# Performance work log

Measured on AMD Instinct MI355X. Metric: run time of the kernel, lower is better.

## Reference

```python
import jax, jax.numpy as jnp
import numpy as np

NUM_FEAT = 10
GAMMA = 1.0
HIDDEN = 30


def setup_inputs() -> dict:
    key = jax.random.key(0)
    ks = jax.random.split(key, 10)
    B, T = 2048, 512
    atom_i = jax.random.randint(ks[0], (B, T), 0, 118, dtype=jnp.int32)
    atom_j = jax.random.randint(ks[1], (B, T), 0, 118, dtype=jnp.int32)
    dist = jax.random.uniform(ks[2], (B, T), minval=0.5, maxval=7.0, dtype=jnp.float32)
    emb = jax.random.normal(ks[3], (118, NUM_FEAT), dtype=jnp.float32)
    s = 1.0 / np.sqrt(HIDDEN)
    W_ih = jax.random.uniform(ks[4], (3 * HIDDEN, NUM_FEAT), minval=-s, maxval=s, dtype=jnp.float32)
    W_hh = jax.random.uniform(ks[5], (3 * HIDDEN, HIDDEN), minval=-s, maxval=s, dtype=jnp.float32)
    b_ih = jax.random.uniform(ks[6], (3 * HIDDEN,), minval=-s, maxval=s, dtype=jnp.float32)
    b_hh = jax.random.uniform(ks[7], (3 * HIDDEN,), minval=-s, maxval=s, dtype=jnp.float32)
    W_out = jax.random.uniform(ks[8], (1, HIDDEN), minval=-s, maxval=s, dtype=jnp.float32)
    b_out = jax.random.uniform(ks[9], (1,), minval=-s, maxval=s, dtype=jnp.float32)
    return dict(atom_i=atom_i, atom_j=atom_j, dist=dist, emb=emb,
                W_ih=W_ih, W_hh=W_hh, b_ih=b_ih, b_hh=b_hh,
                W_out=W_out, b_out=b_out)


def _forward(atom_i, atom_j, dist, emb, W_ih, W_hh, b_ih, b_hh, W_out, b_out):
    B = atom_i.shape[0]
    mask_i = (atom_i != 0)[..., None]  # [B,T,1]
    mask_j = (atom_j != 0)[..., None]
    # conditional embedding gather: index 0 means 'no atom' -> zero vector
    e_i = jnp.where(mask_i, emb[atom_i], 0.0)  # [B,T,10]
    e_j = jnp.where(mask_j, emb[atom_j], 0.0)
    # RBF distance expansion, zeroed where atom_i is absent
    centers = jnp.arange(1, NUM_FEAT + 1, dtype=dist.dtype) * 0.7  # [10]
    rbf = jnp.exp(-GAMMA * (centers - dist[..., None]) ** 2)  # [B,T,10]
    rbf = jnp.where(mask_i, rbf, 0.0)
    feat = jnp.concatenate([e_i, e_j, rbf], axis=-1)  # [B,T,30]
    # view(B,10,-1).permute(0,2,1): row-major reshape then transpose -> [B, 3T, 10]
    x = feat.reshape(B, NUM_FEAT, -1).transpose(0, 2, 1)
    # GRU (batch_first, 1 layer); precompute input projections for all steps
    gi = jnp.einsum('bsd,hd->bsh', x, W_ih) + b_ih  # [B, 3T, 90]

    def step(h, g):
        gh = h @ W_hh.T + b_hh  # [B,90]
        i_r, i_z, i_n = jnp.split(g, 3, axis=-1)
        h_r, h_z, h_n = jnp.split(gh, 3, axis=-1)
        r = jax.nn.sigmoid(i_r + h_r)
        z = jax.nn.sigmoid(i_z + h_z)
        n = jnp.tanh(i_n + r * h_n)
        h = (1.0 - z) * n + z * h
        return h, None

    h0 = jnp.zeros((B, HIDDEN), dtype=x.dtype)
    h_last, _ = jax.lax.scan(step, h0, gi.transpose(1, 0, 2))  # only last step is used
    # dropout is identity in eval mode
    out = jax.nn.relu(h_last @ W_out.T + b_out)  # [B,1]
    return out.squeeze(-1)  # [B]


def reference(atom_i, atom_j, dist, emb, W_ih, W_hh, b_ih, b_hh, W_out, b_out):
    return _forward(atom_i, atom_j, dist, emb, W_ih, W_hh, b_ih, b_hh, W_out, b_out)
```

## Files before the change

kernel.cpp:

```cpp
#include <hip/hip_runtime.h>

#define BATCH 2048
#define T 512
#define NF 10
#define HID 30
#define S3T 1536
#define FEAT_PER_B 15360

typedef float v2f __attribute__((ext_vector_type(2)));

#define LOG2E 1.44269504088896f

__device__ __forceinline__ float fexp(float x) {
    return __builtin_amdgcn_exp2f(x * LOG2E);
}
__device__ __forceinline__ float frcp(float x) {
    return __builtin_amdgcn_rcpf(x);
}

__device__ __forceinline__ v2f pk_fma(v2f a, v2f b, v2f c) {
    v2f d;
    asm("v_pk_fma_f32 %0, %1, %2, %3" : "=v"(d) : "v"(a), "v"(b), "v"(c));
    return d;
}

__global__ void __launch_bounds__(512)
feat_kernel(const int* __restrict__ atom_i,
            const int* __restrict__ atom_j,
            const float* __restrict__ dist,
            const float* __restrict__ emb,
            float4* __restrict__ xpair4) {
    __shared__ float lf[512 * 31 + 30];
    const int b = blockIdx.x;
    const int t = threadIdx.x;

    {
        const int bt = b * T + t;
        const int ai = atom_i[bt];
        const int aj = atom_j[bt];
        const float dd = dist[bt];
        const float mi = (ai != 0) ? 1.0f : 0.0f;
        const float mj = (aj != 0) ? 1.0f : 0.0f;
        const float* ei = &emb[ai * NF];
        const float* ej = &emb[aj * NF];
        float* row = &lf[t * 31];
#pragma unroll
        for (int c = 0; c < NF; ++c) row[c] = mi * ei[c];
#pragma unroll
        for (int c = 0; c < NF; ++c) row[10 + c] = mj * ej[c];
#pragma unroll
        for (int c = 0; c < NF; ++c) {
            float ctr = (float)(c + 1) * 0.7f;
            float df = ctr - dd;
            row[20 + c] = mi * fexp(-df * df);
        }
    }
    __syncthreads();

    float4* ob = xpair4 + (long)b * (FEAT_PER_B / 4);
    for (int o = t; o < FEAT_PER_B / 4; o += 512) {
        unsigned p  = (unsigned)o / 768u;
        unsigned c4 = (unsigned)o - p * 768u;
        float vv[4];
#pragma unroll
        for (int kx = 0; kx < 4; ++kx) {
            unsigned s = 2u * c4 + (unsigned)(kx >> 1);
            unsigned e = (unsigned)(kx & 1);
            unsigned f = (2u * p + e) * 1536u + s;
            unsigned tt = f / 30u;
            unsigned cc = f - tt * 30u;
            vv[kx] = lf[tt * 31u + cc];
        }
        ob[o] = make_float4(vv[0], vv[1], vv[2], vv[3]);
    }
}

#define STEP(PAR, XQ, IDX)                                                   \
    {                                                                        \
        const float4* hv = (const float4*)&hbuf[PAR][half * 32];             \
        v2f hj[16];                                                          \
        _Pragma("unroll")                                                    \
        for (int qq = 0; qq < 8; ++qq) {                                     \
            float4 tq = hv[qq];                                              \
            __builtin_memcpy(&hj[2 * qq], &tq, 16);                          \
        }                                                                    \
        v2f xc[5];                                                           \
        _Pragma("unroll")                                                    \
        for (int pp = 0; pp < 5; ++pp)                                       \
            __builtin_memcpy(&xc[pp], ((const char*)&XQ[pp]) + 8 * (IDX), 8);\
        v2f ar2 = pk_fma(wir[0], xc[0], brv);                                \
        v2f az2 = pk_fma(wiz[0], xc[0], bzv);                                \
        v2f ai2 = pk_fma(win[0], xc[0], biv);                                \
        _Pragma("unroll")                                                    \
        for (int d2 = 1; d2 < 5; ++d2) {                                     \
            ar2 = pk_fma(wir[d2], xc[d2], ar2);                              \
            az2 = pk_fma(wiz[d2], xc[d2], az2);                              \
            ai2 = pk_fma(win[d2], xc[d2], ai2);                              \
        }                                                                    \
        v2f ah2 = pk_fma(whn[0], hj[0], bhv);                                \
        _Pragma("unroll")                                                    \
        for (int j = 0; j < 15; ++j) {                                       \
            ar2 = pk_fma(whr[j], hj[j], ar2);                                \
            az2 = pk_fma(whz[j], hj[j], az2);                                \
            if (j) ah2 = pk_fma(whn[j], hj[j], ah2);                         \
        }                                                                    \
        float ar = ar2.x + ar2.y, az = az2.x + az2.y;                        \
        float ah = ah2.x + ah2.y, ai = ai2.x + ai2.y;                        \
        float er = __builtin_amdgcn_exp2f(ar);                               \
        float ez = __builtin_amdgcn_exp2f(az);                               \
        float rg = frcp(1.0f + er);                                          \
        float zg = frcp(1.0f + ez);                                          \
        float ng =                                                           \
            2.0f * frcp(1.0f + __builtin_amdgcn_exp2f(ai + rg * ah)) - 1.0f; \
        h = ng + zg * (h - ng);                                              \
        hbuf[(PAR) ^ 1][half * 32 + k] = h;                                  \
        __builtin_amdgcn_fence(__ATOMIC_ACQ_REL, "wavefront");               \
    }

__attribute__((amdgpu_waves_per_eu(1, 1)))
__global__ void __launch_bounds__(64)
gru_kernel(const float* __restrict__ xpair,
           const float* __restrict__ W_ih,
           const float* __restrict__ W_hh,
           const float* __restrict__ b_ih,
           const float* __restrict__ b_hh,
           const float* __restrict__ W_out,
           const float* __restrict__ b_out,
           float* __restrict__ out) {
    __shared__ __align__(16) float hbuf[2][64];
    const int lane = threadIdx.x;
    const int half = lane >> 5;
    const int k    = lane & 31;
    const bool active = (k < HID);
    const int kk = active ? k : (HID - 1);
    const int b = blockIdx.x * 2 + half;

    const float SRZ = -LOG2E;
    const float SN  = -2.0f * LOG2E;

    v2f whr[15], whz[15], whn[15];
    {
        const float2* Rr = (const float2*)&W_hh[(0 * HID + kk) * HID];
        const float2* Rz = (const float2*)&W_hh[(1 * HID + kk) * HID];
        const float2* Rn = (const float2*)&W_hh[(2 * HID + kk) * HID];
#pragma unroll
        for (int j = 0; j < 15; ++j) {
            float2 tr = Rr[j], tz = Rz[j], tn = Rn[j];
            whr[j] = (v2f){tr.x * SRZ, tr.y * SRZ};
            whz[j] = (v2f){tz.x * SRZ, tz.y * SRZ};
            whn[j] = (v2f){tn.x * SN,  tn.y * SN};
        }
    }
    v2f wir[5], wiz[5], win[5];
    {
        const float2* Rr = (const float2*)&W_ih[(0 * HID + kk) * NF];
        const float2* Rz = (const float2*)&W_ih[(1 * HID + kk) * NF];
        const float2* Rn = (const float2*)&W_ih[(2 * HID + kk) * NF];
#pragma unroll
        for (int d = 0; d < 5; ++d) {
            float2 tr = Rr[d], tz = Rz[d], tn = Rn[d];
            wir[d] = (v2f){tr.x * SRZ, tr.y * SRZ};
            wiz[d] = (v2f){tz.x * SRZ, tz.y * SRZ};
            win[d] = (v2f){tn.x * SN,  tn.y * SN};
        }
    }
    const v2f brv = (v2f){SRZ * (b_ih[0 * HID + kk] + b_hh[0 * HID + kk]), 0.0f};
    const v2f bzv = (v2f){SRZ * (b_ih[1 * HID + kk] + b_hh[1 * HID + kk]), 0.0f};
    const v2f biv = (v2f){SN * b_ih[2 * HID + kk], 0.0f};
    const v2f bhv = (v2f){SN * b_hh[2 * HID + kk], 0.0f};

    const float* xb = xpair + (long)b * FEAT_PER_B;
    const float4* xa[5];
#pragma unroll
    for (int p = 0; p < 5; ++p) xa[p] = (const float4*)(xb + p * 3072);

    hbuf[0][lane] = 0.0f;
    hbuf[1][lane] = 0.0f;
    __builtin_amdgcn_fence(__ATOMIC_ACQ_REL, "wavefront");

    float h = 0.0f;
    float4 xq0[5], xq1[5];
#pragma unroll
    for (int p = 0; p < 5; ++p) xq0[p] = xa[p][0];

    for (int c2 = 0; c2 < 768; c2 += 2) {
#pragma unroll
        for (int p = 0; p < 5; ++p) xq1[p] = xa[p][c2 + 1];
        STEP(0, xq0, 0);
        STEP(1, xq0, 1);
        const int cn = (c2 + 2 < 768) ? (c2 + 2) : 767;
#pragma unroll
        for (int p = 0; p < 5; ++p) xq0[p] = xa[p][cn];
        STEP(0, xq1, 0);
        STEP(1, xq1, 1);
    }

    float v = active ? h * W_out[kk] : 0.0f;
#pragma unroll
    for (int off = 16; off; off >>= 1) v += __shfl_xor(v, off, 32);
    if (k == 0) {
        float o = v + b_out[0];
        out[b] = o > 0.0f ? o : 0.0f;
    }
}

extern "C" void kernel_launch(void* const* d_in, const int* in_sizes, int n_in,
                              void* d_out, int out_size, void* d_ws, size_t ws_size,
                              hipStream_t stream) {
    const int* atom_i   = (const int*)d_in[0];
    const int* atom_j   = (const int*)d_in[1];
    const float* dist   = (const float*)d_in[2];
    const float* emb    = (const float*)d_in[3];
    const float* W_ih   = (const float*)d_in[4];
    const float* W_hh   = (const float*)d_in[5];
    const float* b_ih   = (const float*)d_in[6];
    const float* b_hh   = (const float*)d_in[7];
    const float* W_out  = (const float*)d_in[8];
    const float* b_out  = (const float*)d_in[9];
    float* out = (float*)d_out;
    float* xpair = (float*)d_ws;

    feat_kernel<<<BATCH, 512, 0, stream>>>(atom_i, atom_j, dist, emb,
                                           (float4*)xpair);
    gru_kernel<<<BATCH / 2, 64, 0, stream>>>(xpair, W_ih, W_hh, b_ih, b_hh,
                                             W_out, b_out, out);
}
```

Baseline: 456.8 us.

## Switch GRU recurrence to fp16 dot2 with fp16 features and hidden state

Stores the intermediate feature tensor as fp16, keeps weights and the shared hidden-state buffer in fp16, and replaces the packed fp32 FMAs with v_dot2 fp16 instructions that accumulate in fp32. This shortens the serial per-step dependency chain: fewer instructions per step, and fewer LDS bytes read for the hidden state. It also halves workspace traffic. In exchange, rounding the hidden state and weights to fp16 at every one of 1536 steps can build up numerical error.

```diff
diff --git a/kernel.cpp b/kernel.cpp
--- a/kernel.cpp
+++ b/kernel.cpp
@@ -7,7 +7,8 @@
 #define S3T 1536
 #define FEAT_PER_B 15360
 
-typedef float v2f __attribute__((ext_vector_type(2)));
+typedef float  v2f __attribute__((ext_vector_type(2)));
+typedef _Float16 v2h __attribute__((ext_vector_type(2)));
 
 #define LOG2E 1.44269504088896f
 
@@ -16,12 +17,6 @@
 }
 __device__ __forceinline__ float frcp(float x) {
     return __builtin_amdgcn_rcpf(x);
-}
-
-__device__ __forceinline__ v2f pk_fma(v2f a, v2f b, v2f c) {
-    v2f d;
-    asm("v_pk_fma_f32 %0, %1, %2, %3" : "=v"(d) : "v"(a), "v"(b), "v"(c));
-    return d;
 }
 
 __global__ void __launch_bounds__(512)
@@ -29,7 +24,7 @@
             const int* __restrict__ atom_j,
             const float* __restrict__ dist,
             const float* __restrict__ emb,
-            float4* __restrict__ xpair4) {
+            uint4* __restrict__ xpair8) {
     __shared__ float lf[512 * 31 + 30];
     const int b = blockIdx.x;
     const int t = threadIdx.x;
@@ -57,55 +52,52 @@
     }
     __syncthreads();
 
-    float4* ob = xpair4 + (long)b * (FEAT_PER_B / 4);
-    for (int o = t; o < FEAT_PER_B / 4; o += 512) {
-        unsigned p  = (unsigned)o / 768u;
-        unsigned c4 = (unsigned)o - p * 768u;
-        float vv[4];
-#pragma unroll
-        for (int kx = 0; kx < 4; ++kx) {
-            unsigned s = 2u * c4 + (unsigned)(kx >> 1);
+    uint4* ob = xpair8 + (long)b * 1920;
+    for (int o = t; o < 1920; o += 512) {
+        unsigned p  = (unsigned)o / 384u;
+        unsigned c4 = (unsigned)o - p * 384u;
+        union { _Float16 h[8]; uint4 u; } pk;
+#pragma unroll
+        for (int kx = 0; kx < 8; ++kx) {
+            unsigned s = 4u * c4 + (unsigned)(kx >> 1);
             unsigned e = (unsigned)(kx & 1);
             unsigned f = (2u * p + e) * 1536u + s;
             unsigned tt = f / 30u;
             unsigned cc = f - tt * 30u;
-            vv[kx] = lf[tt * 31u + cc];
-        }
-        ob[o] = make_float4(vv[0], vv[1], vv[2], vv[3]);
+            pk.h[kx] = (_Float16)lf[tt * 31u + cc];
+        }
+        ob[o] = pk.u;
     }
 }
 
 #define STEP(PAR, XQ, IDX)                                                   \
     {                                                                        \
-        const float4* hv = (const float4*)&hbuf[PAR][half * 32];             \
-        v2f hj[16];                                                          \
+        const uint4* hv = (const uint4*)&hbuf16[PAR][half * 32];             \
+        uint4 t0 = hv[0], t1 = hv[1], t2 = hv[2], t3 = hv[3];                \
+        v2h hj[16];                                                          \
+        __builtin_memcpy(&hj[0], &t0, 16);                                   \
+        __builtin_memcpy(&hj[4], &t1, 16);                                   \
+        __builtin_memcpy(&hj[8], &t2, 16);                                   \
+        __builtin_memcpy(&hj[12], &t3, 16);                                  \
+        v2h xc[5];                                                           \
         _Pragma("unroll")                                                    \
-        for (int qq = 0; qq < 8; ++qq) {                                     \
-            float4 tq = hv[qq];                                              \
-            __builtin_memcpy(&hj[2 * qq], &tq, 16);                          \
+        for (int pp = 0; pp < 5; ++pp) {                                     \
+            unsigned w = ((const unsigned*)&XQ[pp])[IDX];                    \
+            __builtin_memcpy(&xc[pp], &w, 4);                                \
         }                                                                    \
-        v2f xc[5];                                                           \
-        _Pragma("unroll")                                                    \
-        for (int pp = 0; pp < 5; ++pp)                                       \
-            __builtin_memcpy(&xc[pp], ((const char*)&XQ[pp]) + 8 * (IDX), 8);\
-        v2f ar2 = pk_fma(wir[0], xc[0], brv);                                \
-        v2f az2 = pk_fma(wiz[0], xc[0], bzv);                                \
-        v2f ai2 = pk_fma(win[0], xc[0], biv);                                \
-        _Pragma("unroll")                                                    \
-        for (int d2 = 1; d2 < 5; ++d2) {                                     \
-            ar2 = pk_fma(wir[d2], xc[d2], ar2);                              \
-            az2 = pk_fma(wiz[d2], xc[d2], az2);                              \
-            ai2 = pk_fma(win[d2], xc[d2], ai2);                              \
-        }                                                                    \
-        v2f ah2 = pk_fma(whn[0], hj[0], bhv);                                \
+        float ar = brf, az = bzf, ai = bif, ah = bhf;                        \
         _Pragma("unroll")                                                    \
         for (int j = 0; j < 15; ++j) {                                       \
-            ar2 = pk_fma(whr[j], hj[j], ar2);                                \
-            az2 = pk_fma(whz[j], hj[j], az2);                                \
-            if (j) ah2 = pk_fma(whn[j], hj[j], ah2);                         \
+            ar = __builtin_amdgcn_fdot2(whr[j], hj[j], ar, false);           \
+            az = __builtin_amdgcn_fdot2(whz[j], hj[j], az, false);           \
+            ah = __builtin_amdgcn_fdot2(whn[j], hj[j], ah, false);           \
         }                                                                    \
-        float ar = ar2.x + ar2.y, az = az2.x + az2.y;                        \
-        float ah = ah2.x + ah2.y, ai = ai2.x + ai2.y;                        \
+        _Pragma("unroll")                                                    \
+        for (int d = 0; d < 5; ++d) {                                        \
+            ar = __builtin_amdgcn_fdot2(wir[d], xc[d], ar, false);           \
+            az = __builtin_amdgcn_fdot2(wiz[d], xc[d], az, false);           \
+            ai = __builtin_amdgcn_fdot2(win[d], xc[d], ai, false);           \
+        }                                                                    \
         float er = __builtin_amdgcn_exp2f(ar);                               \
         float ez = __builtin_amdgcn_exp2f(az);                               \
         float rg = frcp(1.0f + er);                                          \
@@ -113,13 +105,13 @@
         float ng =                                                           \
             2.0f * frcp(1.0f + __builtin_amdgcn_exp2f(ai + rg * ah)) - 1.0f; \
         h = ng + zg * (h - ng);                                              \
-        hbuf[(PAR) ^ 1][half * 32 + k] = h;                                  \
+        hbuf16[(PAR) ^ 1][half * 32 + k] = (_Float16)h;                      \
         __builtin_amdgcn_fence(__ATOMIC_ACQ_REL, "wavefront");               \
     }
 
 __attribute__((amdgpu_waves_per_eu(1, 1)))
 __global__ void __launch_bounds__(64)
-gru_kernel(const float* __restrict__ xpair,
+gru_kernel(const _Float16* __restrict__ xpair,
            const float* __restrict__ W_ih,
            const float* __restrict__ W_hh,
            const float* __restrict__ b_ih,
@@ -127,7 +119,7 @@
            const float* __restrict__ W_out,
            const float* __restrict__ b_out,
            float* __restrict__ out) {
-    __shared__ __align__(16) float hbuf[2][64];
+    __shared__ __align__(16) _Float16 hbuf16[2][64];
     const int lane = threadIdx.x;
     const int half = lane >> 5;
     const int k    = lane & 31;
@@ -138,7 +130,7 @@
     const float SRZ = -LOG2E;
     const float SN  = -2.0f * LOG2E;
 
-    v2f whr[15], whz[15], whn[15];
+    v2h whr[15], whz[15], whn[15];
     {
         const float2* Rr = (const float2*)&W_hh[(0 * HID + kk) * HID];
         const float2* Rz = (const float2*)&W_hh[(1 * HID + kk) * HID];
@@ -146,12 +138,12 @@
 #pragma unroll
         for (int j = 0; j < 15; ++j) {
             float2 tr = Rr[j], tz = Rz[j], tn = Rn[j];
-            whr[j] = (v2f){tr.x * SRZ, tr.y * SRZ};
-            whz[j] = (v2f){tz.x * SRZ, tz.y * SRZ};
-            whn[j] = (v2f){tn.x * SN,  tn.y * SN};
-        }
-    }
-    v2f wir[5], wiz[5], win[5];
+            whr[j] = (v2h){(_Float16)(tr.x * SRZ), (_Float16)(tr.y * SRZ)};
+            whz[j] = (v2h){(_Float16)(tz.x * SRZ), (_Float16)(tz.y * SRZ)};
+            whn[j] = (v2h){(_Float16)(tn.x * SN),  (_Float16)(tn.y * SN)};
+        }
+    }
+    v2h wir[5], wiz[5], win[5];
     {
         const float2* Rr = (const float2*)&W_ih[(0 * HID + kk) * NF];
         const float2* Rz = (const float2*)&W_ih[(1 * HID + kk) * NF];
@@ -159,40 +151,40 @@
 #pragma unroll
         for (int d = 0; d < 5; ++d) {
             float2 tr = Rr[d], tz = Rz[d], tn = Rn[d];
-            wir[d] = (v2f){tr.x * SRZ, tr.y * SRZ};
-            wiz[d] = (v2f){tz.x * SRZ, tz.y * SRZ};
-            win[d] = (v2f){tn.x * SN,  tn.y * SN};
-        }
-    }
-    const v2f brv = (v2f){SRZ * (b_ih[0 * HID + kk] + b_hh[0 * HID + kk]), 0.0f};
-    const v2f bzv = (v2f){SRZ * (b_ih[1 * HID + kk] + b_hh[1 * HID + kk]), 0.0f};
-    const v2f biv = (v2f){SN * b_ih[2 * HID + kk], 0.0f};
-    const v2f bhv = (v2f){SN * b_hh[2 * HID + kk], 0.0f};
-
-    const float* xb = xpair + (long)b * FEAT_PER_B;
-    const float4* xa[5];
-#pragma unroll
-    for (int p = 0; p < 5; ++p) xa[p] = (const float4*)(xb + p * 3072);
-
-    hbuf[0][lane] = 0.0f;
-    hbuf[1][lane] = 0.0f;
+            wir[d] = (v2h){(_Float16)(tr.x * SRZ), (_Float16)(tr.y * SRZ)};
+            wiz[d] = (v2h){(_Float16)(tz.x * SRZ), (_Float16)(tz.y * SRZ)};
+            win[d] = (v2h){(_Float16)(tn.x * SN),  (_Float16)(tn.y * SN)};
+        }
+    }
+    const float brf = SRZ * (b_ih[0 * HID + kk] + b_hh[0 * HID + kk]);
+    const float bzf = SRZ * (b_ih[1 * HID + kk] + b_hh[1 * HID + kk]);
+    const float bif = SN * b_ih[2 * HID + kk];
+    const float bhf = SN * b_hh[2 * HID + kk];
+
+    const _Float16* xb = xpair + (long)b * FEAT_PER_B;
+    const uint4* xa[5];
+#pragma unroll
+    for (int p = 0; p < 5; ++p) xa[p] = (const uint4*)(xb + p * 3072);
+
+    hbuf16[0][lane] = (_Float16)0.0f;
+    hbuf16[1][lane] = (_Float16)0.0f;
     __builtin_amdgcn_fence(__ATOMIC_ACQ_REL, "wavefront");
 
     float h = 0.0f;
-    float4 xq0[5], xq1[5];
+    uint4 xq0[5], xq1[5];
 #pragma unroll
     for (int p = 0; p < 5; ++p) xq0[p] = xa[p][0];
 
-    for (int c2 = 0; c2 < 768; c2 += 2) {
-#pragma unroll
-        for (int p = 0; p < 5; ++p) xq1[p] = xa[p][c2 + 1];
+    for (int c = 0; c < 384; ++c) {
+        const int cn = (c + 1 < 384) ? (c + 1) : c;
+#pragma unroll
+        for (int p = 0; p < 5; ++p) xq1[p] = xa[p][cn];
         STEP(0, xq0, 0);
         STEP(1, xq0, 1);
-        const int cn = (c2 + 2 < 768) ? (c2 + 2) : 767;
-#pragma unroll
-        for (int p = 0; p < 5; ++p) xq0[p] = xa[p][cn];
-        STEP(0, xq1, 0);
-        STEP(1, xq1, 1);
+        STEP(0, xq0, 2);
+        STEP(1, xq0, 3);
+#pragma unroll
+        for (int p = 0; p < 5; ++p) xq0[p] = xq1[p];
     }
 
     float v = active ? h * W_out[kk] : 0.0f;
@@ -218,10 +210,10 @@
     const float* W_out  = (const float*)d_in[8];
     const float* b_out  = (const float*)d_in[9];
     float* out = (float*)d_out;
-    float* xpair = (float*)d_ws;
+    _Float16* xpair = (_Float16*)d_ws;
 
     feat_kernel<<<BATCH, 512, 0, stream>>>(atom_i, atom_j, dist, emb,
-                                           (float4*)xpair);
+                                           (uint4*)xpair);
     gru_kernel<<<BATCH / 2, 64, 0, stream>>>(xpair, W_ih, W_hh, b_ih, b_hh,
                                              W_out, b_out, out);
 }
```

Result: faster. 402.2 us (-11.9%).
